# Performance work log

Hardware: AMD Instinct MI355X
Metric: run time of the kernel (lower is better)

Reference implementation:

```python
import jax, jax.numpy as jnp
import numpy as np

V, E, H, L = 50257, 512, 512, 2
PAD_ID = 50256


def setup_inputs() -> dict:
    key = jax.random.key(0)
    ks = jax.random.split(key, 24)
    B, TD, TE = 16, 64, 256
    s = 0.02
    emb = jax.random.normal(ks[0], (V, E), jnp.float32) * s
    emb = emb.at[PAD_ID].set(0.0)  # padding_idx row is zero
    inp = {
        "dec_input_ids": jax.random.randint(ks[1], (B, TD), 0, V, jnp.int32),
        "initial_hidden": jax.random.normal(ks[2], (L, B, H), jnp.float32),
        "initial_cell": jax.random.normal(ks[3], (L, B, H), jnp.float32),
        "encoder_outputs": jax.random.normal(ks[4], (B, TE, H), jnp.float32),
        "src_mask": jax.random.randint(ks[5], (B, TE), 0, 2, jnp.int32),
        "emb": emb,
        "W1_w": jax.random.normal(ks[6], (H, H), jnp.float32) * s,
        "W1_b": jnp.zeros((H,), jnp.float32),
        "W2_w": jax.random.normal(ks[7], (H, H), jnp.float32) * s,
        "W2_b": jnp.zeros((H,), jnp.float32),
        "v_w": jax.random.normal(ks[8], (H,), jnp.float32) * s,
        "v_b": jnp.zeros((), jnp.float32),
        "W_ih0": jax.random.normal(ks[9], (4 * H, E + H), jnp.float32) * s,
        "W_hh0": jax.random.normal(ks[10], (4 * H, H), jnp.float32) * s,
        "b_ih0": jnp.zeros((4 * H,), jnp.float32),
        "b_hh0": jnp.zeros((4 * H,), jnp.float32),
        "W_ih1": jax.random.normal(ks[11], (4 * H, H), jnp.float32) * s,
        "W_hh1": jax.random.normal(ks[12], (4 * H, H), jnp.float32) * s,
        "b_ih1": jnp.zeros((4 * H,), jnp.float32),
        "b_hh1": jnp.zeros((4 * H,), jnp.float32),
        "fc_w": jax.random.normal(ks[13], (V, H), jnp.float32) * s,
        "fc_b": jnp.zeros((V,), jnp.float32),
    }
    return inp


def _lstm_cell(x, h, c, Wi, Wh, bi, bh):
    g = x @ Wi.T + bi + h @ Wh.T + bh  # (B, 4H)
    i, f, gg, o = jnp.split(g, 4, axis=-1)  # PyTorch gate order i,f,g,o
    i, f, o = jax.nn.sigmoid(i), jax.nn.sigmoid(f), jax.nn.sigmoid(o)
    gg = jnp.tanh(gg)
    cn = f * c + i * gg
    hn = o * jnp.tanh(cn)
    return hn, cn


def reference(dec_input_ids, initial_hidden, initial_cell, encoder_outputs, src_mask,
              emb, W1_w, W1_b, W2_w, W2_b, v_w, v_b,
              W_ih0, W_hh0, b_ih0, b_hh0, W_ih1, W_hh1, b_ih1, b_hh1,
              fc_w, fc_b):
    embedded = emb[dec_input_ids]                      # (B, T_dec, E)
    enc_proj = encoder_outputs @ W1_w.T + W1_b         # W1(encoder_outputs), (B, T_enc, H)
    pad = src_mask == 0                                # (B, T_enc)
    layers = ((W_ih0, W_hh0, b_ih0, b_hh0), (W_ih1, W_hh1, b_ih1, b_hh1))

    def step(carry, emb_t):
        h, c = carry                                   # each (L, B, H)
        q = h[-1] @ W2_w.T + W2_b                      # (B, H)
        score = jnp.tanh(enc_proj + q[:, None, :]) @ v_w + v_b  # (B, T_enc)
        score = jnp.where(pad, -1e9, score)
        attn = jax.nn.softmax(score, axis=-1)
        context = jnp.einsum('bt,bth->bh', attn, encoder_outputs)
        x = jnp.concatenate([emb_t, context], axis=-1)  # (B, E+H)
        hs, cs = [], []
        for l, (Wi, Wh, bi, bh) in enumerate(layers):
            hn, cn = _lstm_cell(x, h[l], c[l], Wi, Wh, bi, bh)
            hs.append(hn); cs.append(cn)
            x = hn
        logits_t = x @ fc_w.T + fc_b                    # (B, V)
        return (jnp.stack(hs), jnp.stack(cs)), logits_t

    _, logits = jax.lax.scan(step, (initial_hidden, initial_cell),
                             jnp.swapaxes(embedded, 0, 1))  # (T_dec, B, V)
    return jnp.swapaxes(logits, 0, 1)                       # (B, T_dec, V)
```

## Files before the change

### kernel.cpp

```cpp
#include <hip/hip_runtime.h>

#define DI __device__ __forceinline__

typedef __attribute__((ext_vector_type(2))) float f32x2;
typedef __attribute__((ext_vector_type(4))) float f32x4;
typedef __attribute__((ext_vector_type(8))) short bf16x8;
typedef __attribute__((ext_vector_type(8))) unsigned short u16x8;

constexpr int Vv = 50257, NPAD = 50304, Ee = 512, Hh = 512, Bb = 16, TDn = 64, TEn = 256;
constexpr int NBLK = 64;

constexpr size_t OFF_ENCP = 0;
constexpr size_t OFF_ENCT = OFF_ENCP + (size_t)Bb*TEn*Hh*4;
constexpr size_t OFF_G0E  = OFF_ENCT + (size_t)Bb*Hh*TEn*4;
constexpr size_t OFF_FCWB = OFF_G0E  + (size_t)TDn*Bb*4*Hh*4;
constexpr size_t OFF_H1B  = OFF_FCWB + (size_t)NPAD*Hh*2;
constexpr size_t OFF_Q    = OFF_H1B  + (size_t)TDn*Bb*Hh*2;
constexpr size_t OFF_SC   = OFF_Q    + (size_t)Bb*Hh*4;
constexpr size_t OFF_CTX  = OFF_SC   + (size_t)Bb*TEn*4;
constexpr size_t OFF_H0   = OFF_CTX  + (size_t)Bb*Hh*4;
constexpr size_t OFF_H1   = OFF_H0   + (size_t)2*Bb*Hh*4;
constexpr size_t OFF_SYNC = OFF_H1   + (size_t)2*Bb*Hh*4;

DI float dot4(f32x4 a, f32x4 b) { return a[0]*b[0] + a[1]*b[1] + a[2]*b[2] + a[3]*b[3]; }
DI float wsum(float v) { for (int m = 32; m; m >>= 1) v += __shfl_xor(v, m, 64); return v; }
DI float wmax(float v) { for (int m = 32; m; m >>= 1) v = fmaxf(v, __shfl_xor(v, m, 64)); return v; }
DI void wsum4(float& a, float& b, float& c, float& d) {
    #pragma unroll
    for (int m = 32; m; m >>= 1) {
        a += __shfl_xor(a, m, 64);
        b += __shfl_xor(b, m, 64);
        c += __shfl_xor(c, m, 64);
        d += __shfl_xor(d, m, 64);
    }
}
DI float tanhfast(float x) { float e = __expf(2.f * x); return 1.f - 2.f / (e + 1.f); }
DI float sigm(float x) { return 1.f / (1.f + __expf(-x)); }

DI int swz(int a) { return a ^ (((a >> 5) & 7) << 2); }

DI float gload1(const float* p) {
    return __hip_atomic_load(p, __ATOMIC_RELAXED, __HIP_MEMORY_SCOPE_AGENT);
}
DI void gstore1(float* p, float v) {
    __hip_atomic_store(p, v, __ATOMIC_RELAXED, __HIP_MEMORY_SCOPE_AGENT);
}
DI f32x2 gload2(const float* p) {
    unsigned long long u = __hip_atomic_load((const unsigned long long*)p,
                                             __ATOMIC_RELAXED, __HIP_MEMORY_SCOPE_AGENT);
    return __builtin_bit_cast(f32x2, u);
}
DI void gstore2(float* p, f32x2 v) {
    __hip_atomic_store((unsigned long long*)p, __builtin_bit_cast(unsigned long long, v),
                       __ATOMIC_RELAXED, __HIP_MEMORY_SCOPE_AGENT);
}
DI f32x4 gload4(const float* p) {
    f32x2 a = gload2(p), b = gload2(p + 2);
    f32x4 r; r[0] = a[0]; r[1] = a[1]; r[2] = b[0]; r[3] = b[1];
    return r;
}
DI void gstoreu16(unsigned short* p, unsigned short v) {
    __hip_atomic_store(p, v, __ATOMIC_RELAXED, __HIP_MEMORY_SCOPE_AGENT);
}

DI unsigned short f2bf(float f) {
    unsigned u = __builtin_bit_cast(unsigned, f);
    unsigned r = (u + 0x7FFFu + ((u >> 16) & 1u)) >> 16;
    return (unsigned short)r;
}
DI u16x8 cvt8(f32x4 a, f32x4 b) {
    u16x8 r;
    r[0]=f2bf(a[0]); r[1]=f2bf(a[1]); r[2]=f2bf(a[2]); r[3]=f2bf(a[3]);
    r[4]=f2bf(b[0]); r[5]=f2bf(b[1]); r[6]=f2bf(b[2]); r[7]=f2bf(b[3]);
    return r;
}

DI void gbar(char* sy, int bid, unsigned kg) {
    __syncthreads();
    const size_t pofs = (kg & 1) ? 0 : 1024;
    unsigned long long* arr = (unsigned long long*)(sy + pofs);
    unsigned* gen = (unsigned*)(sy + 2048 + pofs);
    const int tid = threadIdx.x;
    if (tid == 0) {
        asm volatile("s_waitcnt vmcnt(0)" ::: "memory");
        char* p = (char*)(arr + (size_t)(bid >> 3) * 16) + (bid & 7);
        __hip_atomic_store(p, (char)(unsigned char)kg, __ATOMIC_RELAXED, __HIP_MEMORY_SCOPE_AGENT);
    }
    if (bid == 0) {
        if (tid < 64) {
            const unsigned long long pat = 0x0101010101010101ULL * (unsigned char)kg;
            for (;;) {
                bool ok = true;
                if (tid < 8)
                    ok = (__hip_atomic_load(arr + (size_t)tid * 16, __ATOMIC_RELAXED,
                                            __HIP_MEMORY_SCOPE_AGENT) == pat);
                if (__all(ok)) break;
                __builtin_amdgcn_s_sleep(2);
            }
            asm volatile("" ::: "memory");
            if (tid < 8)
                __hip_atomic_store(gen + (size_t)tid * 32, kg, __ATOMIC_RELAXED,
                                   __HIP_MEMORY_SCOPE_AGENT);
        }
    } else if (tid == 0) {
        unsigned* gp = gen + (size_t)(bid & 7) * 32;
        while (__hip_atomic_load(gp, __ATOMIC_RELAXED, __HIP_MEMORY_SCOPE_AGENT) != kg)
            __builtin_amdgcn_s_sleep(2);
    }
    __syncthreads();
}

DI void rbar(char* sy, int gb, int u4, unsigned kr) {
    __syncthreads();
    if (threadIdx.x == 0) {
        const size_t pofs = (kr & 1) ? 4096 : 6144;
        unsigned* w = (unsigned*)(sy + pofs) + (size_t)gb * 32;
        asm volatile("s_waitcnt vmcnt(0)" ::: "memory");
        __hip_atomic_store((char*)w + u4, (char)(unsigned char)kr, __ATOMIC_RELAXED,
                           __HIP_MEMORY_SCOPE_AGENT);
        const unsigned pat = 0x01010101u * (unsigned char)kr;
        while (__hip_atomic_load(w, __ATOMIC_RELAXED, __HIP_MEMORY_SCOPE_AGENT) != pat)
            __builtin_amdgcn_s_sleep(2);
    }
    __syncthreads();
}

__global__ void prep_fcw_kernel(const float* __restrict__ src, unsigned short* __restrict__ dst) {
    size_t i = ((size_t)blockIdx.x * 256 + threadIdx.x) << 3;
    int n = (int)(i >> 9);
    u16x8 v = {0,0,0,0,0,0,0,0};
    if (n < Vv) {
        const float* p = src + i;
        v = cvt8(*(const f32x4*)p, *(const f32x4*)(p + 4));
    }
    *(u16x8*)(dst + i) = v;
}

__global__ void transpose_kernel(const float* __restrict__ enc, float* __restrict__ encT) {
    __shared__ float tile[32][33];
    const int b = blockIdx.z, e0 = blockIdx.x << 5, h0 = blockIdx.y << 5;
    const int tx = threadIdx.x, ty = threadIdx.y;
    #pragma unroll
    for (int i = 0; i < 4; ++i)
        tile[ty + i*8][tx] = enc[((size_t)(b*TEn + e0 + ty + i*8))*Hh + h0 + tx];
    __syncthreads();
    #pragma unroll
    for (int i = 0; i < 4; ++i)
        encT[((size_t)(b*Hh + h0 + ty + i*8))*TEn + e0 + tx] = tile[tx][ty + i*8];
}

template<int SRCBF, int GATHER, int OUTM>
__global__ __launch_bounds__(256, 2) void gemm_bt(
    const void* __restrict__ Av, const void* __restrict__ Bv,
    const float* __restrict__ bias, const float* __restrict__ bias2,
    float* __restrict__ Cout, int M, int N, int K, int ldb,
    const int* __restrict__ ids, int NV)
{
    __shared__ unsigned short As[128*32], Bs[128*32];
    const int tid = threadIdx.x;
    const int bn = blockIdx.x, bm = blockIdx.y;
    const int w = tid >> 6, l = tid & 63;
    const int wm = w >> 1, wn = w & 1;
    const int lr = l & 15, ls = l >> 4;
    f32x4 acc[4][4] = {};

    const int r0 = tid >> 2, c0 = (tid & 3) << 3;

    for (int kb = 0; kb < K; kb += 32) {
        #pragma unroll
        for (int half = 0; half < 2; ++half) {
            const int rr = r0 + half*64;
            {
                const int gm = bm*128 + rr;
                size_t arow = GATHER ? (size_t)ids[((gm & 15) << 6) + (gm >> 4)] : (size_t)gm;
                u16x8 v;
                if (SRCBF) {
                    v = *(const u16x8*)((const unsigned short*)Av + arow*(size_t)K + kb + c0);
                } else {
                    const float* ap = (const float*)Av + arow*(size_t)K + kb + c0;
                    v = cvt8(*(const f32x4*)ap, *(const f32x4*)(ap + 4));
                }
                *(u16x8*)&As[rr*32 + c0] = v;
            }
            {
                const size_t brow = (size_t)(bn*128 + rr);
                u16x8 v;
                if (SRCBF) {
                    v = *(const u16x8*)((const unsigned short*)Bv + brow*(size_t)ldb + kb + c0);
                } else {
                    const float* bp = (const float*)Bv + brow*(size_t)ldb + kb + c0;
                    v = cvt8(*(const f32x4*)bp, *(const f32x4*)(bp + 4));
                }
                *(u16x8*)&Bs[rr*32 + c0] = v;
            }
        }
        __syncthreads();
        bf16x8 af[4], bfv[4];
        #pragma unroll
        for (int mt = 0; mt < 4; ++mt) af[mt]  = *(const bf16x8*)&As[(wm*64 + mt*16 + lr)*32 + ls*8];
        #pragma unroll
        for (int nt = 0; nt < 4; ++nt) bfv[nt] = *(const bf16x8*)&Bs[(wn*64 + nt*16 + lr)*32 + ls*8];
        #pragma unroll
        for (int mt = 0; mt < 4; ++mt)
            #pragma unroll
            for (int nt = 0; nt < 4; ++nt)
                acc[mt][nt] = __builtin_amdgcn_mfma_f32_16x16x32_bf16(af[mt], bfv[nt], acc[mt][nt], 0, 0, 0);
        __syncthreads();
    }

    #pragma unroll
    for (int mt = 0; mt < 4; ++mt) {
        #pragma unroll
        for (int nt = 0; nt < 4; ++nt) {
            const int n = bn*128 + wn*64 + nt*16 + lr;
            const int mbase = bm*128 + wm*64 + mt*16 + ls*4;
            f32x4 a = acc[mt][nt];
            #pragma unroll
            for (int r = 0; r < 4; ++r) {
                const int m = mbase + r;
                if (OUTM == 0) {
                    float v = a[r] + bias[n] + (bias2 ? bias2[n] : 0.f);
                    Cout[(size_t)m*N + n] = v;
                } else {
                    if (n < NV) {
                        float v = a[r] + bias[n];
                        Cout[(size_t)(((m & 15) << 6) + (m >> 4))*NV + n] = v;
                    }
                }
            }
        }
    }
}

__global__ __launch_bounds__(512, 1) void recur_kernel(
    const float* __restrict__ ih, const float* __restrict__ ic,
    const float* __restrict__ W2w, const float* __restrict__ W2b,
    const float* __restrict__ vw, const float* __restrict__ vb,
    const int* __restrict__ smask,
    const float* __restrict__ Wi0, const float* __restrict__ Wh0,
    const float* __restrict__ Wi1, const float* __restrict__ Wh1,
    const float* __restrict__ bi1, const float* __restrict__ bh1,
    char* __restrict__ ws)
{
    float* encP = (float*)(ws + OFF_ENCP);
    float* encT = (float*)(ws + OFF_ENCT);
    float* g0e  = (float*)(ws + OFF_G0E);
    unsigned short* h1bf = (unsigned short*)(ws + OFF_H1B);
    float* qb  = (float*)(ws + OFF_Q);
    float* sc  = (float*)(ws + OFF_SC);
    float* ctx = (float*)(ws + OFF_CTX);
    float* h0b = (float*)(ws + OFF_H0);
    float* h1v = (float*)(ws + OFF_H1);
    char* sy   = (char*)(ws + OFF_SYNC);

    __shared__ float lds[2 * Bb * Hh];

    const int tid = threadIdx.x, bid = blockIdx.x;
    const int wid = tid >> 6, l = tid & 63;
    const int j  = (bid << 3) + wid;
    const int k0 = l << 3;

    f32x4 wi0a[4], wi0b[4], wh0a[4], wh0b[4];
    f32x4 wi1a[4], wi1b[4], wh1a[4], wh1b[4];
    float bb1[4];
    #pragma unroll
    for (int g = 0; g < 4; ++g) {
        const float* p0 = Wi0 + (size_t)(g*Hh + j)*(Ee + Hh) + Ee + k0;
        wi0a[g] = *(const f32x4*)p0; wi0b[g] = *(const f32x4*)(p0 + 4);
        const float* p1 = Wh0 + (size_t)(g*Hh + j)*Hh + k0;
        wh0a[g] = *(const f32x4*)p1; wh0b[g] = *(const f32x4*)(p1 + 4);
        const float* p2 = Wi1 + (size_t)(g*Hh + j)*Hh + k0;
        wi1a[g] = *(const f32x4*)p2; wi1b[g] = *(const f32x4*)(p2 + 4);
        const float* p3 = Wh1 + (size_t)(g*Hh + j)*Hh + k0;
        wh1a[g] = *(const f32x4*)p3; wh1b[g] = *(const f32x4*)(p3 + 4);
        bb1[g] = bi1[g*Hh + j] + bh1[g*Hh + j];
    }
    const float* wr = W2w + (size_t)j*Hh + k0;
    const f32x4 w2a = *(const f32x4*)wr, w2d = *(const f32x4*)(wr + 4);
    const float w2bias = W2b[j];
    const f32x4 va = *(const f32x4*)&vw[k0], vd = *(const f32x4*)&vw[k0 + 4];
    const float vbias = vb[0];

    float c0r = (l < 16) ? ic[l*Hh + j]           : 0.f;
    float c1r = (l < 16) ? ic[Bb*Hh + l*Hh + j]   : 0.f;

    const int gb  = bid & 15, u4 = bid >> 4;
    const int se0 = u4*64 + wid*8;
    const int ch0 = u4*128 + wid*16;
    const int msk = (l < 8) ? smask[gb*TEn + se0 + l] : 1;

    for (int i = (bid*512 + tid)*4; i < Bb*Hh; i += NBLK*512*4) {
        gstore2(&h0b[i],     *(const f32x2*)&ih[i]);
        gstore2(&h0b[i + 2], *(const f32x2*)&ih[i + 2]);
        gstore2(&h1v[i],     *(const f32x2*)&ih[Bb*Hh + i]);
        gstore2(&h1v[i + 2], *(const f32x2*)&ih[Bb*Hh + i + 2]);
    }
    unsigned kg = 1, kr = 0;
    gbar(sy, bid, kg);

    for (int t = 0; t < TDn; ++t) {
        const int p = t & 1;
        const float* h1r = h1v + p*(Bb*Hh);
        float*       h1w = h1v + (p^1)*(Bb*Hh);
        const float* h0r = h0b + p*(Bb*Hh);
        float*       h0w = h0b + (p^1)*(Bb*Hh);

        float ge0 = 0.f, ge1 = 0.f, ge2 = 0.f, ge3 = 0.f;
        if (l < 16) {
            const float* gp = g0e + ((size_t)(t*Bb + l))*(4*Hh) + j;
            ge0 = gp[0]; ge1 = gp[Hh]; ge2 = gp[2*Hh]; ge3 = gp[3*Hh];
        }

        {
            for (int i = tid*4; i < Bb*Hh; i += 2048)
                *(f32x4*)&lds[swz(i)] = gload4(&h1r[i]);
            __syncthreads();
            float qv = 0.f;
            #pragma unroll 4
            for (int b = 0; b < Bb; ++b) {
                f32x4 ha = *(const f32x4*)&lds[swz(b*Hh + k0)];
                f32x4 hd = *(const f32x4*)&lds[swz(b*Hh + k0 + 4)];
                float s = dot4(ha, w2a) + dot4(hd, w2d);
                s = wsum(s);
                qv = (l == b) ? s + w2bias : qv;
            }
            if (l < 16) gstore1(&qb[l*Hh + j], qv);
        }
        gbar(sy, bid, ++kg);

        {
            if (tid < 128) *(f32x4*)&lds[tid*4] = gload4(&qb[gb*Hh + tid*4]);
            __syncthreads();
            f32x4 qa = *(const f32x4*)&lds[k0];
            f32x4 qd = *(const f32x4*)&lds[k0 + 4];
            float myS = 0.f;
            #pragma unroll
            for (int i = 0; i < 8; ++i) {
                const int e = se0 + i;
                const float* ep = encP + ((size_t)(gb*TEn + e))*Hh + k0;
                f32x4 ea = *(const f32x4*)ep, ed = *(const f32x4*)(ep + 4);
                float s = 0.f;
                #pragma unroll
                for (int c = 0; c < 4; ++c)
                    s += tanhfast(ea[c] + qa[c]) * va[c] + tanhfast(ed[c] + qd[c]) * vd[c];
                s = wsum(s);
                myS = (l == i) ? s : myS;
            }
            if (l < 8)
                gstore1(&sc[gb*TEn + se0 + l], (msk == 0) ? -1e9f : (myS + vbias));
        }
        rbar(sy, gb, u4, ++kr);

        {
            f32x4 s4 = gload4(&sc[gb*TEn + (l << 2)]);
            float mx = wmax(fmaxf(fmaxf(s4[0], s4[1]), fmaxf(s4[2], s4[3])));
            f32x4 e4; float sm = 0.f;
            #pragma unroll
            for (int c = 0; c < 4; ++c) { e4[c] = __expf(s4[c] - mx); sm += e4[c]; }
            sm = wsum(sm);
            const float inv = 1.0f / sm;
            float myC = 0.f;
            #pragma unroll 4
            for (int i = 0; i < 16; ++i) {
                const int h = ch0 + i;
                f32x4 en = *(const f32x4*)&encT[((size_t)(gb*Hh + h))*TEn + (l << 2)];
                float s = wsum(dot4(e4, en));
                myC = (l == i) ? s : myC;
            }
            if (l < 16) gstore1(&ctx[gb*Hh + ch0 + l], myC * inv);
        }
        gbar(sy, bid, ++kg);

        {
            for (int i = tid*4; i < Bb*Hh; i += 2048) {
                *(f32x4*)&lds[swz(i)]          = gload4(&ctx[i]);
                *(f32x4*)&lds[swz(Bb*Hh + i)]  = gload4(&h0r[i]);
            }
            __syncthreads();
            float ls0 = 0.f, ls1 = 0.f, ls2 = 0.f, ls3 = 0.f;
            #pragma unroll 4
            for (int b = 0; b < Bb; ++b) {
                f32x4 xa = *(const f32x4*)&lds[swz(b*Hh + k0)];
                f32x4 xd = *(const f32x4*)&lds[swz(b*Hh + k0 + 4)];
                f32x4 ha = *(const f32x4*)&lds[swz(Bb*Hh + b*Hh + k0)];
                f32x4 hd = *(const f32x4*)&lds[swz(Bb*Hh + b*Hh + k0 + 4)];
                float s0 = dot4(wi0a[0],xa)+dot4(wi0b[0],xd)+dot4(wh0a[0],ha)+dot4(wh0b[0],hd);
                float s1 = dot4(wi0a[1],xa)+dot4(wi0b[1],xd)+dot4(wh0a[1],ha)+dot4(wh0b[1],hd);
                float s2 = dot4(wi0a[2],xa)+dot4(wi0b[2],xd)+dot4(wh0a[2],ha)+dot4(wh0b[2],hd);
                float s3 = dot4(wi0a[3],xa)+dot4(wi0b[3],xd)+dot4(wh0a[3],ha)+dot4(wh0b[3],hd);
                wsum4(s0, s1, s2, s3);
                if (l == b) { ls0 = s0; ls1 = s1; ls2 = s2; ls3 = s3; }
            }
            if (l < 16) {
                float ii = sigm(ls0 + ge0), ff = sigm(ls1 + ge1);
                float gg = tanhfast(ls2 + ge2), oo = sigm(ls3 + ge3);
                float cn = ff*c0r + ii*gg;
                c0r = cn;
                gstore1(&h0w[l*Hh + j], oo * tanhfast(cn));
            }
        }
        gbar(sy, bid, ++kg);

        {
            for (int i = tid*4; i < Bb*Hh; i += 2048) {
                *(f32x4*)&lds[swz(i)]          = gload4(&h0w[i]);
                *(f32x4*)&lds[swz(Bb*Hh + i)]  = gload4(&h1r[i]);
            }
            __syncthreads();
            float ls0 = 0.f, ls1 = 0.f, ls2 = 0.f, ls3 = 0.f;
            #pragma unroll 4
            for (int b = 0; b < Bb; ++b) {
                f32x4 xa = *(const f32x4*)&lds[swz(b*Hh + k0)];
                f32x4 xd = *(const f32x4*)&lds[swz(b*Hh + k0 + 4)];
                f32x4 ha = *(const f32x4*)&lds[swz(Bb*Hh + b*Hh + k0)];
                f32x4 hd = *(const f32x4*)&lds[swz(Bb*Hh + b*Hh + k0 + 4)];
                float s0 = dot4(wi1a[0],xa)+dot4(wi1b[0],xd)+dot4(wh1a[0],ha)+dot4(wh1b[0],hd);
                float s1 = dot4(wi1a[1],xa)+dot4(wi1b[1],xd)+dot4(wh1a[1],ha)+dot4(wh1b[1],hd);
                float s2 = dot4(wi1a[2],xa)+dot4(wi1b[2],xd)+dot4(wh1a[2],ha)+dot4(wh1b[2],hd);
                float s3 = dot4(wi1a[3],xa)+dot4(wi1b[3],xd)+dot4(wh1a[3],ha)+dot4(wh1b[3],hd);
                wsum4(s0, s1, s2, s3);
                if (l == b) { ls0 = s0; ls1 = s1; ls2 = s2; ls3 = s3; }
            }
            if (l < 16) {
                float ii = sigm(ls0 + bb1[0]), ff = sigm(ls1 + bb1[1]);
                float gg = tanhfast(ls2 + bb1[2]), oo = sigm(ls3 + bb1[3]);
                float cn = ff*c1r + ii*gg;
                c1r = cn;
                float hn = oo * tanhfast(cn);
                gstore1(&h1w[l*Hh + j], hn);
                gstoreu16(&h1bf[((size_t)(t*Bb + l))*Hh + j], f2bf(hn));
            }
        }
        gbar(sy, bid, ++kg);
    }
}

extern "C" void kernel_launch(void* const* d_in, const int* in_sizes, int n_in,
                              void* d_out, int out_size, void* d_ws, size_t ws_size,
                              hipStream_t stream)
{
    const int*   ids  = (const int*)d_in[0];
    const float* ih   = (const float*)d_in[1];
    const float* ic   = (const float*)d_in[2];
    const float* enc  = (const float*)d_in[3];
    const int*   smask= (const int*)d_in[4];
    const float* emb  = (const float*)d_in[5];
    const float* W1w  = (const float*)d_in[6];
    const float* W1b  = (const float*)d_in[7];
    const float* W2w  = (const float*)d_in[8];
    const float* W2b  = (const float*)d_in[9];
    const float* vw   = (const float*)d_in[10];
    const float* vb   = (const float*)d_in[11];
    const float* Wi0  = (const float*)d_in[12];
    const float* Wh0  = (const float*)d_in[13];
    const float* bi0  = (const float*)d_in[14];
    const float* bh0  = (const float*)d_in[15];
    const float* Wi1  = (const float*)d_in[16];
    const float* Wh1  = (const float*)d_in[17];
    const float* bi1  = (const float*)d_in[18];
    const float* bh1  = (const float*)d_in[19];
    const float* fcw  = (const float*)d_in[20];
    const float* fcb  = (const float*)d_in[21];
    float* out = (float*)d_out;
    char*  ws  = (char*)d_ws;

    hipMemsetAsync(ws + OFF_SYNC, 0, 8192, stream);

    prep_fcw_kernel<<<dim3((unsigned)((size_t)NPAD*Hh/8/256)), dim3(256), 0, stream>>>(
        fcw, (unsigned short*)(ws + OFF_FCWB));

    transpose_kernel<<<dim3(TEn/32, Hh/32, Bb), dim3(32, 8), 0, stream>>>(
        enc, (float*)(ws + OFF_ENCT));

    gemm_bt<0,0,0><<<dim3(Hh/128, (Bb*TEn)/128), dim3(256), 0, stream>>>(
        enc, W1w, W1b, nullptr, (float*)(ws + OFF_ENCP),
        Bb*TEn, Hh, Hh, Hh, nullptr, 0);

    gemm_bt<0,1,0><<<dim3((4*Hh)/128, (TDn*Bb)/128), dim3(256), 0, stream>>>(
        emb, Wi0, bi0, bh0, (float*)(ws + OFF_G0E),
        TDn*Bb, 4*Hh, Ee, Ee + Hh, ids, 0);

    {
        void* args[] = { (void*)&ih, (void*)&ic, (void*)&W2w, (void*)&W2b,
                         (void*)&vw, (void*)&vb, (void*)&smask,
                         (void*)&Wi0, (void*)&Wh0, (void*)&Wi1, (void*)&Wh1,
                         (void*)&bi1, (void*)&bh1, (void*)&ws };
        hipLaunchCooperativeKernel((void*)recur_kernel, dim3(NBLK), dim3(512), args, 0, stream);
    }

    gemm_bt<1,0,1><<<dim3(NPAD/128, (TDn*Bb)/128), dim3(256), 0, stream>>>(
        ws + OFF_H1B, ws + OFF_FCWB, fcb, nullptr, out,
        TDn*Bb, NPAD, Hh, Hh, nullptr, Vv);
}
```

Before: 3.181 ms.

## Use transpose-reduce across lanes and flat all-to-all grid barrier in recurrent kernel

```diff
diff --git a/kernel.cpp b/kernel.cpp
--- a/kernel.cpp
+++ b/kernel.cpp
@@ -25,17 +25,33 @@
 DI float dot4(f32x4 a, f32x4 b) { return a[0]*b[0] + a[1]*b[1] + a[2]*b[2] + a[3]*b[3]; }
 DI float wsum(float v) { for (int m = 32; m; m >>= 1) v += __shfl_xor(v, m, 64); return v; }
 DI float wmax(float v) { for (int m = 32; m; m >>= 1) v = fmaxf(v, __shfl_xor(v, m, 64)); return v; }
-DI void wsum4(float& a, float& b, float& c, float& d) {
-    #pragma unroll
-    for (int m = 32; m; m >>= 1) {
-        a += __shfl_xor(a, m, 64);
-        b += __shfl_xor(b, m, 64);
-        c += __shfl_xor(c, m, 64);
-        d += __shfl_xor(d, m, 64);
-    }
-}
 DI float tanhfast(float x) { float e = __expf(2.f * x); return 1.f - 2.f / (e + 1.f); }
 DI float sigm(float x) { return 1.f / (1.f + __expf(-x)); }
+
+template<int NV>
+DI float xreduce(float (&buf)[NV], const int l) {
+    int cnt = NV;
+    #pragma unroll
+    for (int m = 1; m < NV; m <<= 1) {
+        const bool hi = (l & m) != 0;
+        #pragma unroll
+        for (int i = 0; i < NV; ++i) {
+            if (i < cnt / 2) {
+                float x0 = buf[2*i], x1 = buf[2*i + 1];
+                float send = hi ? x0 : x1;
+                float keep = hi ? x1 : x0;
+                float recv = __shfl_xor(send, m, 64);
+                buf[i] = keep + recv;
+            }
+        }
+        cnt >>= 1;
+    }
+    float v = buf[0];
+    #pragma unroll
+    for (int m = NV; m < 64; m <<= 1)
+        v += __shfl_xor(v, m, 64);
+    return v;
+}
 
 DI int swz(int a) { return a ^ (((a >> 5) & 7) << 2); }
 
@@ -77,35 +93,21 @@
 
 DI void gbar(char* sy, int bid, unsigned kg) {
     __syncthreads();
-    const size_t pofs = (kg & 1) ? 0 : 1024;
-    unsigned long long* arr = (unsigned long long*)(sy + pofs);
-    unsigned* gen = (unsigned*)(sy + 2048 + pofs);
+    unsigned* fl = (unsigned*)(sy + ((kg & 1) ? 0 : 8192));
     const int tid = threadIdx.x;
     if (tid == 0) {
         asm volatile("s_waitcnt vmcnt(0)" ::: "memory");
-        char* p = (char*)(arr + (size_t)(bid >> 3) * 16) + (bid & 7);
-        __hip_atomic_store(p, (char)(unsigned char)kg, __ATOMIC_RELAXED, __HIP_MEMORY_SCOPE_AGENT);
-    }
-    if (bid == 0) {
-        if (tid < 64) {
-            const unsigned long long pat = 0x0101010101010101ULL * (unsigned char)kg;
-            for (;;) {
-                bool ok = true;
-                if (tid < 8)
-                    ok = (__hip_atomic_load(arr + (size_t)tid * 16, __ATOMIC_RELAXED,
-                                            __HIP_MEMORY_SCOPE_AGENT) == pat);
-                if (__all(ok)) break;
-                __builtin_amdgcn_s_sleep(2);
-            }
-            asm volatile("" ::: "memory");
-            if (tid < 8)
-                __hip_atomic_store(gen + (size_t)tid * 32, kg, __ATOMIC_RELAXED,
-                                   __HIP_MEMORY_SCOPE_AGENT);
-        }
-    } else if (tid == 0) {
-        unsigned* gp = gen + (size_t)(bid & 7) * 32;
-        while (__hip_atomic_load(gp, __ATOMIC_RELAXED, __HIP_MEMORY_SCOPE_AGENT) != kg)
-            __builtin_amdgcn_s_sleep(2);
+        __hip_atomic_store(fl + (size_t)bid * 32, kg, __ATOMIC_RELAXED, __HIP_MEMORY_SCOPE_AGENT);
+    }
+    if (tid < 64) {
+        bool done = false;
+        for (;;) {
+            if (!done)
+                done = (__hip_atomic_load(fl + (size_t)tid * 32, __ATOMIC_RELAXED,
+                                          __HIP_MEMORY_SCOPE_AGENT) == kg);
+            if (__all(done)) break;
+            __builtin_amdgcn_s_sleep(32);
+        }
     }
     __syncthreads();
 }
@@ -113,14 +115,13 @@
 DI void rbar(char* sy, int gb, int u4, unsigned kr) {
     __syncthreads();
     if (threadIdx.x == 0) {
-        const size_t pofs = (kr & 1) ? 4096 : 6144;
-        unsigned* w = (unsigned*)(sy + pofs) + (size_t)gb * 32;
+        unsigned* w = (unsigned*)(sy + ((kr & 1) ? 16384 : 18432)) + (size_t)gb * 32;
         asm volatile("s_waitcnt vmcnt(0)" ::: "memory");
         __hip_atomic_store((char*)w + u4, (char)(unsigned char)kr, __ATOMIC_RELAXED,
                            __HIP_MEMORY_SCOPE_AGENT);
         const unsigned pat = 0x01010101u * (unsigned char)kr;
         while (__hip_atomic_load(w, __ATOMIC_RELAXED, __HIP_MEMORY_SCOPE_AGENT) != pat)
-            __builtin_amdgcn_s_sleep(2);
+            __builtin_amdgcn_s_sleep(8);
     }
     __syncthreads();
 }
@@ -232,7 +233,7 @@
     }
 }
 
-__global__ __launch_bounds__(512, 1) void recur_kernel(
+__global__ __launch_bounds__(512, 2) void recur_kernel(
     const float* __restrict__ ih, const float* __restrict__ ic,
     const float* __restrict__ W2w, const float* __restrict__ W2b,
     const float* __restrict__ vw, const float* __restrict__ vb,
@@ -281,8 +282,13 @@
     const f32x4 va = *(const f32x4*)&vw[k0], vd = *(const f32x4*)&vw[k0 + 4];
     const float vbias = vb[0];
 
-    float c0r = (l < 16) ? ic[l*Hh + j]           : 0.f;
-    float c1r = (l < 16) ? ic[Bb*Hh + l*Hh + j]   : 0.f;
+    const bool cellLane = ((l & 3) == 0) && (l < 32);
+    const int  bA = l >> 2;
+    float c0r[2], c1r[2];
+    c0r[0] = cellLane ? ic[bA*Hh + j]              : 0.f;
+    c0r[1] = cellLane ? ic[(8 + bA)*Hh + j]        : 0.f;
+    c1r[0] = cellLane ? ic[Bb*Hh + bA*Hh + j]      : 0.f;
+    c1r[1] = cellLane ? ic[Bb*Hh + (8 + bA)*Hh + j]: 0.f;
 
     const int gb  = bid & 15, u4 = bid >> 4;
     const int se0 = u4*64 + wid*8;
@@ -305,25 +311,26 @@
         const float* h0r = h0b + p*(Bb*Hh);
         float*       h0w = h0b + (p^1)*(Bb*Hh);
 
-        float ge0 = 0.f, ge1 = 0.f, ge2 = 0.f, ge3 = 0.f;
-        if (l < 16) {
-            const float* gp = g0e + ((size_t)(t*Bb + l))*(4*Hh) + j;
-            ge0 = gp[0]; ge1 = gp[Hh]; ge2 = gp[2*Hh]; ge3 = gp[3*Hh];
+        float ge[2][4] = {};
+        if (cellLane) {
+            const float* gpA = g0e + ((size_t)(t*Bb + bA))*(4*Hh) + j;
+            const float* gpB = g0e + ((size_t)(t*Bb + 8 + bA))*(4*Hh) + j;
+            #pragma unroll
+            for (int g = 0; g < 4; ++g) { ge[0][g] = gpA[(size_t)g*Hh]; ge[1][g] = gpB[(size_t)g*Hh]; }
         }
 
         {
             for (int i = tid*4; i < Bb*Hh; i += 2048)
                 *(f32x4*)&lds[swz(i)] = gload4(&h1r[i]);
             __syncthreads();
-            float qv = 0.f;
-            #pragma unroll 4
+            float a[16];
+            #pragma unroll
             for (int b = 0; b < Bb; ++b) {
                 f32x4 ha = *(const f32x4*)&lds[swz(b*Hh + k0)];
                 f32x4 hd = *(const f32x4*)&lds[swz(b*Hh + k0 + 4)];
-                float s = dot4(ha, w2a) + dot4(hd, w2d);
-                s = wsum(s);
-                qv = (l == b) ? s + w2bias : qv;
-            }
+                a[b] = dot4(ha, w2a) + dot4(hd, w2d);
+            }
+            float qv = xreduce<16>(a, l) + w2bias;
             if (l < 16) gstore1(&qb[l*Hh + j], qv);
         }
         gbar(sy, bid, ++kg);
@@ -333,21 +340,20 @@
             __syncthreads();
             f32x4 qa = *(const f32x4*)&lds[k0];
             f32x4 qd = *(const f32x4*)&lds[k0 + 4];
-            float myS = 0.f;
+            float a[8];
             #pragma unroll
             for (int i = 0; i < 8; ++i) {
-                const int e = se0 + i;
-                const float* ep = encP + ((size_t)(gb*TEn + e))*Hh + k0;
+                const float* ep = encP + ((size_t)(gb*TEn + se0 + i))*Hh + k0;
                 f32x4 ea = *(const f32x4*)ep, ed = *(const f32x4*)(ep + 4);
                 float s = 0.f;
                 #pragma unroll
                 for (int c = 0; c < 4; ++c)
                     s += tanhfast(ea[c] + qa[c]) * va[c] + tanhfast(ed[c] + qd[c]) * vd[c];
-                s = wsum(s);
-                myS = (l == i) ? s : myS;
-            }
+                a[i] = s;
+            }
+            float sv = xreduce<8>(a, l) + vbias;
             if (l < 8)
-                gstore1(&sc[gb*TEn + se0 + l], (msk == 0) ? -1e9f : (myS + vbias));
+                gstore1(&sc[gb*TEn + se0 + l], (msk == 0) ? -1e9f : sv);
         }
         rbar(sy, gb, u4, ++kr);
 
@@ -359,15 +365,14 @@
             for (int c = 0; c < 4; ++c) { e4[c] = __expf(s4[c] - mx); sm += e4[c]; }
             sm = wsum(sm);
             const float inv = 1.0f / sm;
-            float myC = 0.f;
-            #pragma unroll 4
+            float a[16];
+            #pragma unroll
             for (int i = 0; i < 16; ++i) {
-                const int h = ch0 + i;
-                f32x4 en = *(const f32x4*)&encT[((size_t)(gb*Hh + h))*TEn + (l << 2)];
-                float s = wsum(dot4(e4, en));
-                myC = (l == i) ? s : myC;
-            }
-            if (l < 16) gstore1(&ctx[gb*Hh + ch0 + l], myC * inv);
+                f32x4 en = *(const f32x4*)&encT[((size_t)(gb*Hh + ch0 + i))*TEn + (l << 2)];
+                a[i] = dot4(e4, en);
+            }
+            float cv = xreduce<16>(a, l) * inv;
+            if (l < 16) gstore1(&ctx[gb*Hh + ch0 + l], cv);
         }
         gbar(sy, bid, ++kg);
 
@@ -377,26 +382,36 @@
                 *(f32x4*)&lds[swz(Bb*Hh + i)]  = gload4(&h0r[i]);
             }
             __syncthreads();
-            float ls0 = 0.f, ls1 = 0.f, ls2 = 0.f, ls3 = 0.f;
-            #pragma unroll 4
-            for (int b = 0; b < Bb; ++b) {
-                f32x4 xa = *(const f32x4*)&lds[swz(b*Hh + k0)];
-                f32x4 xd = *(const f32x4*)&lds[swz(b*Hh + k0 + 4)];
-                f32x4 ha = *(const f32x4*)&lds[swz(Bb*Hh + b*Hh + k0)];
-                f32x4 hd = *(const f32x4*)&lds[swz(Bb*Hh + b*Hh + k0 + 4)];
-                float s0 = dot4(wi0a[0],xa)+dot4(wi0b[0],xd)+dot4(wh0a[0],ha)+dot4(wh0b[0],hd);
-                float s1 = dot4(wi0a[1],xa)+dot4(wi0b[1],xd)+dot4(wh0a[1],ha)+dot4(wh0b[1],hd);
-                float s2 = dot4(wi0a[2],xa)+dot4(wi0b[2],xd)+dot4(wh0a[2],ha)+dot4(wh0b[2],hd);
-                float s3 = dot4(wi0a[3],xa)+dot4(wi0b[3],xd)+dot4(wh0a[3],ha)+dot4(wh0b[3],hd);
-                wsum4(s0, s1, s2, s3);
-                if (l == b) { ls0 = s0; ls1 = s1; ls2 = s2; ls3 = s3; }
-            }
-            if (l < 16) {
-                float ii = sigm(ls0 + ge0), ff = sigm(ls1 + ge1);
-                float gg = tanhfast(ls2 + ge2), oo = sigm(ls3 + ge3);
-                float cn = ff*c0r + ii*gg;
-                c0r = cn;
-                gstore1(&h0w[l*Hh + j], oo * tanhfast(cn));
+            #pragma unroll
+            for (int pass = 0; pass < 2; ++pass) {
+                const int base = pass * 8;
+                float acc[32];
+                #pragma unroll
+                for (int bb = 0; bb < 8; ++bb) {
+                    const int b = base + bb;
+                    f32x4 xa = *(const f32x4*)&lds[swz(b*Hh + k0)];
+                    f32x4 xd = *(const f32x4*)&lds[swz(b*Hh + k0 + 4)];
+                    f32x4 ha = *(const f32x4*)&lds[swz(Bb*Hh + b*Hh + k0)];
+                    f32x4 hd = *(const f32x4*)&lds[swz(Bb*Hh + b*Hh + k0 + 4)];
+                    #pragma unroll
+                    for (int g = 0; g < 4; ++g)
+                        acc[bb*4 + g] = dot4(wi0a[g],xa) + dot4(wi0b[g],xd)
+                                      + dot4(wh0a[g],ha) + dot4(wh0b[g],hd);
+                }
+                float v  = xreduce<32>(acc, l);
+                float x1 = __shfl_xor(v, 1, 64);
+                float x2 = __shfl_xor(v, 2, 64);
+                float x3 = __shfl_xor(v, 3, 64);
+                if (cellLane) {
+                    const int b = base + bA;
+                    float ii = sigm(v  + ge[pass][0]);
+                    float ff = sigm(x1 + ge[pass][1]);
+                    float gg = tanhfast(x2 + ge[pass][2]);
+                    float oo = sigm(x3 + ge[pass][3]);
+                    float cn = ff*c0r[pass] + ii*gg;
+                    c0r[pass] = cn;
+                    gstore1(&h0w[b*Hh + j], oo * tanhfast(cn));
+                }
             }
         }
         gbar(sy, bid, ++kg);
@@ -407,28 +422,38 @@
                 *(f32x4*)&lds[swz(Bb*Hh + i)]  = gload4(&h1r[i]);
             }
             __syncthreads();
-            float ls0 = 0.f, ls1 = 0.f, ls2 = 0.f, ls3 = 0.f;
-            #pragma unroll 4
-            for (int b = 0; b < Bb; ++b) {
-                f32x4 xa = *(const f32x4*)&lds[swz(b*Hh + k0)];
-                f32x4 xd = *(const f32x4*)&lds[swz(b*Hh + k0 + 4)];
-                f32x4 ha = *(const f32x4*)&lds[swz(Bb*Hh + b*Hh + k0)];
-                f32x4 hd = *(const f32x4*)&lds[swz(Bb*Hh + b*Hh + k0 + 4)];
-                float s0 = dot4(wi1a[0],xa)+dot4(wi1b[0],xd)+dot4(wh1a[0],ha)+dot4(wh1b[0],hd);
-                float s1 = dot4(wi1a[1],xa)+dot4(wi1b[1],xd)+dot4(wh1a[1],ha)+dot4(wh1b[1],hd);
-                float s2 = dot4(wi1a[2],xa)+dot4(wi1b[2],xd)+dot4(wh1a[2],ha)+dot4(wh1b[2],hd);
-                float s3 = dot4(wi1a[3],xa)+dot4(wi1b[3],xd)+dot4(wh1a[3],ha)+dot4(wh1b[3],hd);
-                wsum4(s0, s1, s2, s3);
-                if (l == b) { ls0 = s0; ls1 = s1; ls2 = s2; ls3 = s3; }
-            }
-            if (l < 16) {
-                float ii = sigm(ls0 + bb1[0]), ff = sigm(ls1 + bb1[1]);
-                float gg = tanhfast(ls2 + bb1[2]), oo = sigm(ls3 + bb1[3]);
-                float cn = ff*c1r + ii*gg;
-                c1r = cn;
-                float hn = oo * tanhfast(cn);
-                gstore1(&h1w[l*Hh + j], hn);
-                gstoreu16(&h1bf[((size_t)(t*Bb + l))*Hh + j], f2bf(hn));
+            #pragma unroll
+            for (int pass = 0; pass < 2; ++pass) {
+                const int base = pass * 8;
+                float acc[32];
+                #pragma unroll
+                for (int bb = 0; bb < 8; ++bb) {
+                    const int b = base + bb;
+                    f32x4 xa = *(const f32x4*)&lds[swz(b*Hh + k0)];
+                    f32x4 xd = *(const f32x4*)&lds[swz(b*Hh + k0 + 4)];
+                    f32x4 ha = *(const f32x4*)&lds[swz(Bb*Hh + b*Hh + k0)];
+                    f32x4 hd = *(const f32x4*)&lds[swz(Bb*Hh + b*Hh + k0 + 4)];
+                    #pragma unroll
+                    for (int g = 0; g < 4; ++g)
+                        acc[bb*4 + g] = dot4(wi1a[g],xa) + dot4(wi1b[g],xd)
+                                      + dot4(wh1a[g],ha) + dot4(wh1b[g],hd);
+                }
+                float v  = xreduce<32>(acc, l);
+                float x1 = __shfl_xor(v, 1, 64);
+                float x2 = __shfl_xor(v, 2, 64);
+                float x3 = __shfl_xor(v, 3, 64);
+                if (cellLane) {
+                    const int b = base + bA;
+                    float ii = sigm(v  + bb1[0]);
+                    float ff = sigm(x1 + bb1[1]);
+                    float gg = tanhfast(x2 + bb1[2]);
+                    float oo = sigm(x3 + bb1[3]);
+                    float cn = ff*c1r[pass] + ii*gg;
+                    c1r[pass] = cn;
+                    float hn = oo * tanhfast(cn);
+                    gstore1(&h1w[b*Hh + j], hn);
+                    gstoreu16(&h1bf[((size_t)(t*Bb + b))*Hh + j], f2bf(hn));
+                }
             }
         }
         gbar(sy, bid, ++kg);
@@ -464,7 +489,7 @@
     float* out = (float*)d_out;
     char*  ws  = (char*)d_ws;
 
-    hipMemsetAsync(ws + OFF_SYNC, 0, 8192, stream);
+    hipMemsetAsync(ws + OFF_SYNC, 0, 20480, stream);
 
     prep_fcw_kernel<<<dim3((unsigned)((size_t)NPAD*Hh/8/256)), dim3(256), 0, stream>>>(
         fcw, (unsigned short*)(ws + OFF_FCWB));
```

Measured after the change: 3.579 ms. 1.13x slower.
